# Kernel tuning notes

Measured on AMD Instinct MI355X. Metric: run time of the kernel, lower is better.

Reference implementation:

```python
import jax, jax.numpy as jnp
import numpy as np

N = 10000          # num nodes
E = 160000         # num edges (avg degree 16)
F = 128            # num_features
S = 4              # num_species
RAD = 8            # radial_embedding_dim
RO = 16            # readout_mlp_irreps = 16x0e
EPS = 0.17677669529663687  # epsilon = 1/sqrt(avg_degree)
ACT_NORM = 1.679177        # normalize_function(silu): 1/sqrt(E[silu(x)^2]), x~N(0,1)


def nsilu(x):
    return jax.nn.silu(x) * ACT_NORM


def setup_inputs() -> dict:
    key = jax.random.key(0)
    ks = jax.random.split(key, 24)
    d = {}
    d["vectors"] = jax.random.normal(ks[0], (E, 3), jnp.float32)
    d["node_scalars"] = jax.random.normal(ks[1], (N, F), jnp.float32)
    d["node_vectors"] = jax.random.normal(ks[2], (N, F, 3), jnp.float32)
    d["radial_embeddings"] = jax.random.normal(ks[3], (E, RAD), jnp.float32)
    # linear_up (irrep-wise linear on 0e and 1o)
    d["W_up_s"] = jax.random.normal(ks[4], (F, F), jnp.float32)
    d["W_up_v"] = jax.random.normal(ks[5], (F, F), jnp.float32)
    # radial MLP [RAD,64,64,64,weight_dim=4F]
    d["W_mlp1"] = jax.random.normal(ks[6], (RAD, 64), jnp.float32) / np.sqrt(RAD)
    d["b_mlp1"] = jnp.zeros((64,), jnp.float32)
    d["W_mlp2"] = jax.random.normal(ks[7], (64, 64), jnp.float32) / np.sqrt(64.0)
    d["b_mlp2"] = jnp.zeros((64,), jnp.float32)
    d["W_mlp3"] = jax.random.normal(ks[8], (64, 64), jnp.float32) / np.sqrt(64.0)
    d["b_mlp3"] = jnp.zeros((64,), jnp.float32)
    d["W_mlp4"] = jax.random.normal(ks[9], (64, 4 * F), jnp.float32) / np.sqrt(64.0)
    d["b_mlp4"] = jnp.zeros((4 * F,), jnp.float32)
    # linear_down: TP out (2F x 0e + 2F x 1o) -> F x (0e+1o)
    d["W_down_s"] = jax.random.normal(ks[10], (2 * F, F), jnp.float32)
    d["W_down_v"] = jax.random.normal(ks[11], (2 * F, F), jnp.float32)
    # species-indexed skip linear (output is hidden_out = 0e only, since last=True)
    d["Wz_s"] = jax.random.normal(ks[12], (S, F, F), jnp.float32)
    # symmetric contraction weights: 5 invariant basis terms per channel per species
    d["W_sc"] = jax.random.normal(ks[13], (S, 5, F), jnp.float32)
    d["W_post"] = jax.random.normal(ks[14], (F, F), jnp.float32)
    d["W_ro1"] = jax.random.normal(ks[15], (F, RO), jnp.float32)
    d["W_ro2"] = jax.random.normal(ks[16], (RO, 1), jnp.float32)
    d["senders"] = jax.random.randint(ks[17], (E,), 0, N)
    d["receivers"] = jax.random.randint(ks[18], (E,), 0, N)
    d["num_species_counts"] = jnp.full((S,), N // S, dtype=jnp.int32)
    d["num_nodes"] = N
    return d


def reference(vectors, node_scalars, node_vectors, radial_embeddings,
              W_up_s, W_up_v,
              W_mlp1, b_mlp1, W_mlp2, b_mlp2, W_mlp3, b_mlp3, W_mlp4, b_mlp4,
              W_down_s, W_down_v, Wz_s, W_sc, W_post, W_ro1, W_ro2,
              senders, receivers, num_species_counts, num_nodes):
    # spherical harmonics (max_ell=1): Y0 = 1, Y1 = unit edge vector
    rnorm = jnp.linalg.norm(vectors, axis=-1, keepdims=True)
    Y1 = vectors / (rnorm + 1e-12)                      # [E,3]

    # species index per node from counts
    i = jnp.repeat(jnp.arange(S), num_species_counts, total_repeat_length=num_nodes)

    # self connection (species-indexed linear on input scalars; hidden_out = 0e)
    self_conn = jnp.einsum('nf,nfg->ng', node_scalars, Wz_s[i]) / np.sqrt(F)

    # linear_up (irrep-wise)
    s = node_scalars @ W_up_s / np.sqrt(F)              # [N,F]
    v = jnp.einsum('nfc,fg->ngc', node_vectors, W_up_v) / np.sqrt(F)  # [N,F,3]

    # radial MLP -> per-edge channelwise TP weights, 4 paths x F channels
    h = nsilu(radial_embeddings @ W_mlp1 + b_mlp1)
    h = nsilu(h @ W_mlp2 + b_mlp2)
    h = nsilu(h @ W_mlp3 + b_mlp3)
    mix = (h @ W_mlp4 + b_mlp4).reshape(-1, 4, F)       # [E,4,F]

    # channelwise tensor product: gather sender feats, combine with sph
    sg = s[senders]                                     # [E,F]
    vg = v[senders]                                     # [E,F,3]
    m_s0 = mix[:, 0] * sg                               # 0e x 0e -> 0e
    m_s3 = mix[:, 3] * (jnp.einsum('efc,ec->ef', vg, Y1) / np.sqrt(3.0))  # 1o x 1o -> 0e
    m_v1 = mix[:, 1][..., None] * sg[..., None] * Y1[:, None, :]          # 0e x 1o -> 1o
    m_v2 = mix[:, 2][..., None] * vg                                      # 1o x 0e -> 1o
    msg_s = jnp.concatenate([m_s0, m_s3], axis=-1)      # [E,2F]
    msg_v = jnp.concatenate([m_v1, m_v2], axis=1)       # [E,2F,3]

    # scatter to receivers
    agg_s = jax.ops.segment_sum(msg_s, receivers, num_segments=num_nodes) * EPS
    agg_v = jax.ops.segment_sum(msg_v, receivers, num_segments=num_nodes) * EPS

    # linear_down: 2F -> F per irrep
    s2 = agg_s @ W_down_s / np.sqrt(2 * F)              # [N,F]
    v2 = jnp.einsum('nfc,fg->ngc', agg_v, W_down_v) / np.sqrt(2 * F)  # [N,F,3]

    # symmetric contraction (correlation<=3, output 0e): per-species weighted
    # invariant basis {s, s^2, |v|^2, s^3, s|v|^2} per channel
    vv = jnp.sum(v2 * v2, axis=-1)                      # [N,F]
    basis = jnp.stack([s2, s2 * s2, vv, s2 * s2 * s2, s2 * vv], axis=1)  # [N,5,F]
    sc = jnp.sum(W_sc[i] * basis, axis=1)               # [N,F]

    feats = sc @ W_post / np.sqrt(F) + self_conn        # [N,F]

    # readout (last=True): linear -> scalar activation -> linear
    hr = nsilu(feats @ W_ro1 / np.sqrt(F))              # [N,16]
    node_outputs = hr @ W_ro2 / np.sqrt(RO)             # [N,1]
    return (node_outputs, feats)
```

## Files before the change

kernel.cpp:

```cpp
#include <hip/hip_runtime.h>
#include <hip/hip_bf16.h>
#include <math.h>

#define N_NODES 10000
#define N_EDGES 160000
#define F 128
#define TE 128
#define HS 72

typedef _Float16 v8h __attribute__((ext_vector_type(8)));
typedef _Float16 v4h __attribute__((ext_vector_type(4)));
typedef float    v4f __attribute__((ext_vector_type(4)));

__device__ __forceinline__ float nsilu(float x) {
    return 1.679177f * (x / (1.0f + expf(-x)));
}

__device__ __forceinline__ void fma4(float4& a, float s, const float4& b) {
    a.x = fmaf(s, b.x, a.x); a.y = fmaf(s, b.y, a.y);
    a.z = fmaf(s, b.z, a.z); a.w = fmaf(s, b.w, a.w);
}

__device__ __forceinline__ int species_of(int n, const int* __restrict__ counts) {
    int c0 = counts[0];
    int c01 = c0 + counts[1];
    int c012 = c01 + counts[2];
    return (n >= c0) + (n >= c01) + (n >= c012);
}

__global__ __launch_bounds__(256) void k_count(const int* __restrict__ receivers,
                                               int* __restrict__ deg) {
    int e = blockIdx.x * 256 + threadIdx.x;
    if (e < N_EDGES) atomicAdd(&deg[receivers[e]], 1);
}

__global__ __launch_bounds__(1024) void k_scan(const int* __restrict__ deg,
                                               int* __restrict__ offs,
                                               int* __restrict__ cursor) {
    __shared__ int sums[1024];
    const int t = threadIdx.x;
    const int CH = 10;
    int base = t * CH;
    int local[CH];
    int s = 0;
    #pragma unroll
    for (int j = 0; j < CH; ++j) {
        int v = (base + j < N_NODES) ? deg[base + j] : 0;
        local[j] = s;
        s += v;
    }
    sums[t] = s;
    __syncthreads();
    for (int off = 1; off < 1024; off <<= 1) {
        int v = (t >= off) ? sums[t - off] : 0;
        __syncthreads();
        sums[t] += v;
        __syncthreads();
    }
    int carry = (t == 0) ? 0 : sums[t - 1];
    #pragma unroll
    for (int j = 0; j < CH; ++j) {
        int idx = base + j;
        if (idx < N_NODES) {
            int o = carry + local[j];
            offs[idx] = o;
            cursor[idx] = o;
        }
    }
    if (t == 1023) offs[N_NODES] = sums[1023];
}

__global__ __launch_bounds__(256) void k_fill(const int* __restrict__ receivers,
                                              int* __restrict__ cursor,
                                              int* __restrict__ eidx,
                                              float* __restrict__ vectors) {
    int e = blockIdx.x * 256 + threadIdx.x;
    if (e < N_EDGES) {
        int pos = atomicAdd(&cursor[receivers[e]], 1);
        eidx[pos] = e;
        float vx = vectors[e * 3 + 0];
        float vy = vectors[e * 3 + 1];
        float vz = vectors[e * 3 + 2];
        float rn = sqrtf(vx * vx + vy * vy + vz * vz) + 1e-12f;
        float inv = 1.0f / rn;
        vectors[e * 3 + 0] = vx * inv;
        vectors[e * 3 + 1] = vy * inv;
        vectors[e * 3 + 2] = vz * inv;
    }
}

__global__ __launch_bounds__(256) void k_prep_w(
    const float* __restrict__ W2, const float* __restrict__ W3,
    const float* __restrict__ W4, const float* __restrict__ b4,
    const float* __restrict__ Wup_s, const float* __restrict__ Wup_v,
    const float* __restrict__ Wz, const float* __restrict__ Wds,
    const float* __restrict__ Wdv, const float* __restrict__ Wpost,
    _Float16* __restrict__ W2t, _Float16* __restrict__ W3t,
    _Float16* __restrict__ W4t, float* __restrict__ b4p,
    _Float16* __restrict__ Wup_s_t, _Float16* __restrict__ Wup_v_t,
    _Float16* __restrict__ Wz_t, _Float16* __restrict__ Wds_t,
    _Float16* __restrict__ Wdv_t, _Float16* __restrict__ Wpost_t)
{
    int idx = blockIdx.x * 256 + threadIdx.x;
    if (idx < 4096) {
        int u = idx >> 6, k = idx & 63;
        W2t[idx] = (_Float16)W2[k * 64 + u];
    } else if (idx < 8192) {
        int j = idx - 4096;
        int u = j >> 6, k = j & 63;
        W3t[j] = (_Float16)W3[k * 64 + u];
    } else if (idx < 40960) {
        int j = idx - 8192;
        int gn = j >> 6, k = j & 63;
        int go = (gn & 3) * 128 + (gn >> 2);
        W4t[j] = (_Float16)W4[k * 512 + go];
    } else if (idx < 41472) {
        int j = idx - 40960;
        int go = (j & 3) * 128 + (j >> 2);
        b4p[j] = b4[go];
    } else if (idx < 57856) {
        int j = idx - 41472;
        int g = j >> 7, f = j & 127;
        Wup_s_t[j] = (_Float16)Wup_s[f * 128 + g];
    } else if (idx < 74240) {
        int j = idx - 57856;
        int g = j >> 7, f = j & 127;
        Wup_v_t[j] = (_Float16)Wup_v[f * 128 + g];
    } else if (idx < 139776) {
        int j = idx - 74240;
        int s = j >> 14, r = j & 16383;
        int g = r >> 7, f = r & 127;
        Wz_t[j] = (_Float16)Wz[s * 16384 + f * 128 + g];
    } else if (idx < 172544) {
        int j = idx - 139776;
        int g = j >> 8, k = j & 255;
        Wds_t[j] = (_Float16)Wds[k * 128 + g];
    } else if (idx < 205312) {
        int j = idx - 172544;
        int g = j >> 8, k = j & 255;
        Wdv_t[j] = (_Float16)Wdv[k * 128 + g];
    } else if (idx < 221696) {
        int j = idx - 205312;
        int g = j >> 7, f = j & 127;
        Wpost_t[j] = (_Float16)Wpost[f * 128 + g];
    }
}

__global__ __launch_bounds__(256) void k_prep_a(
    const float* __restrict__ ns, const float* __restrict__ nv,
    _Float16* __restrict__ ns16, _Float16* __restrict__ nv16)
{
    int idx = blockIdx.x * 256 + threadIdx.x;
    if (idx < N_NODES * F) {
        ns16[idx] = (_Float16)ns[idx];
    } else {
        int j = idx - N_NODES * F;
        int row = j >> 7, f = j & 127;
        int n = row / 3, c = row - n * 3;
        nv16[j] = (_Float16)nv[((size_t)n * F + f) * 3 + c];
    }
}

template <int K>
__device__ __forceinline__ void gemm_tile(
    const _Float16* __restrict__ A, const _Float16* __restrict__ Bg,
    float* __restrict__ out, int M, int row0, float scale,
    _Float16* Bl, const int* __restrict__ counts, int sp)
{
    const int t = threadIdx.x;
    constexpr int KP = K + 8;
    __syncthreads();
    for (int idx = t; idx < 128 * (K / 8); idx += 256) {
        int g = idx / (K / 8), kk = (idx % (K / 8)) * 8;
        *(v8h*)(Bl + g * KP + kk) = *(const v8h*)(Bg + g * K + kk);
    }
    __syncthreads();

    const int lane = t & 63;
    const int w = t >> 6;
    const int c = lane & 15;
    const int q = lane >> 4;

    v4f acc[2][8];
    #pragma unroll
    for (int mi = 0; mi < 2; ++mi)
        #pragma unroll
        for (int nt = 0; nt < 8; ++nt)
            acc[mi][nt] = (v4f){0.f, 0.f, 0.f, 0.f};

    for (int ch = 0; ch < K / 32; ++ch) {
        v8h a[2];
        #pragma unroll
        for (int mi = 0; mi < 2; ++mi) {
            int r = row0 + (2 * w + mi) * 16 + c;
            r = min(r, M - 1);
            a[mi] = *(const v8h*)(A + (size_t)r * K + ch * 32 + q * 8);
        }
        #pragma unroll
        for (int nt = 0; nt < 8; ++nt) {
            v8h b = *(const v8h*)(Bl + (nt * 16 + c) * KP + ch * 32 + q * 8);
            acc[0][nt] = __builtin_amdgcn_mfma_f32_16x16x32_f16(a[0], b, acc[0][nt], 0, 0, 0);
            acc[1][nt] = __builtin_amdgcn_mfma_f32_16x16x32_f16(a[1], b, acc[1][nt], 0, 0, 0);
        }
    }
    #pragma unroll
    for (int mi = 0; mi < 2; ++mi) {
        #pragma unroll
        for (int r = 0; r < 4; ++r) {
            int row = row0 + (2 * w + mi) * 16 + q * 4 + r;
            bool ok = row < M;
            if (ok && sp >= 0) ok = (species_of(row, counts) == sp);
            if (ok) {
                float* op = out + (size_t)row * 128;
                #pragma unroll
                for (int nt = 0; nt < 8; ++nt)
                    op[nt * 16 + c] = acc[mi][nt][r] * scale;
            }
        }
    }
}

__global__ __launch_bounds__(256) void k_gemm_up(
    const _Float16* __restrict__ ns16, const _Float16* __restrict__ nv16,
    const _Float16* __restrict__ Wup_s_t, const _Float16* __restrict__ Wup_v_t,
    const _Float16* __restrict__ Wz_t, const int* __restrict__ counts,
    float* __restrict__ s_buf, float* __restrict__ v_buf, float* __restrict__ selfc)
{
    __shared__ _Float16 Bl[128 * 136];
    const int row0 = blockIdx.x * 128;
    const float isf = 0.08838834764831845f;
    if (blockIdx.y == 0) {
        if (row0 >= N_NODES) return;
        gemm_tile<128>(ns16, Wup_s_t, s_buf, N_NODES, row0, isf, Bl, counts, -1);
    } else if (blockIdx.y == 1) {
        gemm_tile<128>(nv16, Wup_v_t, v_buf, 3 * N_NODES, row0, isf, Bl, counts, -1);
    } else {
        if (row0 >= N_NODES) return;
        int sp0 = species_of(row0, counts);
        int sp1 = species_of(min(row0 + 127, N_NODES - 1), counts);
        for (int sp = sp0; sp <= sp1; ++sp)
            gemm_tile<128>(ns16, Wz_t + (size_t)sp * 16384, selfc,
                           N_NODES, row0, isf, Bl, counts, sp);
    }
}

__global__ __launch_bounds__(256) void k_gemm_down(
    const _Float16* __restrict__ agg_s16, const _Float16* __restrict__ agg_v16,
    const _Float16* __restrict__ Wds_t, const _Float16* __restrict__ Wdv_t,
    const int* __restrict__ counts,
    float* __restrict__ s2, float* __restrict__ v2)
{
    __shared__ _Float16 Bl[128 * 264];
    const int row0 = blockIdx.x * 128;
    if (blockIdx.y == 0) {
        if (row0 >= N_NODES) return;
        gemm_tile<256>(agg_s16, Wds_t, s2, N_NODES, row0, 1.0f, Bl, counts, -1);
    } else {
        gemm_tile<256>(agg_v16, Wdv_t, v2, 3 * N_NODES, row0, 1.0f, Bl, counts, -1);
    }
}

__device__ __forceinline__ void mfma_layer64(
    const _Float16* src, _Float16* dst,
    const _Float16* __restrict__ Wt, const float* __restrict__ b,
    int w, int q, int c)
{
    v8h B[4][2];
    float bias[4];
    #pragma unroll
    for (int nt = 0; nt < 4; ++nt) {
        B[nt][0] = *(const v8h*)(Wt + (nt * 16 + c) * 64 + q * 8);
        B[nt][1] = *(const v8h*)(Wt + (nt * 16 + c) * 64 + 32 + q * 8);
        bias[nt] = b[nt * 16 + c];
    }
    #pragma unroll
    for (int mi = 0; mi < 2; ++mi) {
        int mt = 2 * w + mi;
        v8h a0 = *(const v8h*)(src + (mt * 16 + c) * HS + q * 8);
        v8h a1 = *(const v8h*)(src + (mt * 16 + c) * HS + 32 + q * 8);
        #pragma unroll
        for (int nt = 0; nt < 4; ++nt) {
            v4f acc = {bias[nt], bias[nt], bias[nt], bias[nt]};
            acc = __builtin_amdgcn_mfma_f32_16x16x32_f16(a0, B[nt][0], acc, 0, 0, 0);
            acc = __builtin_amdgcn_mfma_f32_16x16x32_f16(a1, B[nt][1], acc, 0, 0, 0);
            #pragma unroll
            for (int r = 0; r < 4; ++r)
                dst[(mt * 16 + q * 4 + r) * HS + nt * 16 + c] = (_Float16)nsilu(acc[r]);
        }
    }
}

__global__ __launch_bounds__(256) void k_mlp(
    const float* __restrict__ re,
    const float* __restrict__ W1, const float* __restrict__ b1,
    const _Float16* __restrict__ W2t, const float* __restrict__ b2,
    const _Float16* __restrict__ W3t, const float* __restrict__ b3,
    const _Float16* __restrict__ W4t, const float* __restrict__ b4p,
    _Float16* __restrict__ mix)
{
    __shared__ float sre[TE * 8];
    __shared__ _Float16 hA[TE * HS];
    __shared__ _Float16 hB[TE * HS];

    const int t = threadIdx.x;
    const int e0 = blockIdx.x * TE;

    ((float4*)sre)[t] = ((const float4*)(re + (size_t)e0 * 8))[t];
    __syncthreads();

    {
        const int uslot = t & 15;
        const int egrp = t >> 4;
        const int u0 = uslot * 4;
        float4 w[8];
        #pragma unroll
        for (int k = 0; k < 8; ++k) w[k] = *(const float4*)(W1 + k * 64 + u0);
        float4 bb = *(const float4*)(b1 + u0);
        #pragma unroll
        for (int i = 0; i < 8; ++i) {
            int e = egrp + i * 16;
            const float* rp = sre + e * 8;
            float4 a = bb;
            #pragma unroll
            for (int k = 0; k < 8; ++k) fma4(a, rp[k], w[k]);
            v4h r = {(_Float16)nsilu(a.x), (_Float16)nsilu(a.y),
                     (_Float16)nsilu(a.z), (_Float16)nsilu(a.w)};
            *(v4h*)(hA + e * HS + u0) = r;
        }
    }
    __syncthreads();

    const int lane = t & 63;
    const int w = t >> 6;
    const int c = lane & 15;
    const int q = lane >> 4;

    mfma_layer64(hA, hB, W2t, b2, w, q, c);
    mfma_layer64(hB, hA, W3t, b3, w, q, c);
    __syncthreads();

    v8h B4[8][2];
    float bias4[8];
    #pragma unroll
    for (int j = 0; j < 8; ++j) {
        int g = (8 * w + j) * 16 + c;
        B4[j][0] = *(const v8h*)(W4t + g * 64 + q * 8);
        B4[j][1] = *(const v8h*)(W4t + g * 64 + 32 + q * 8);
        bias4[j] = b4p[g];
    }
    for (int mt = 0; mt < 8; ++mt) {
        v8h a0 = *(const v8h*)(hA + (mt * 16 + c) * HS + q * 8);
        v8h a1 = *(const v8h*)(hA + (mt * 16 + c) * HS + 32 + q * 8);
        size_t rowbase = (size_t)(e0 + mt * 16 + q * 4) * 512;
        #pragma unroll
        for (int j = 0; j < 8; ++j) {
            v4f acc = {bias4[j], bias4[j], bias4[j], bias4[j]};
            acc = __builtin_amdgcn_mfma_f32_16x16x32_f16(a0, B4[j][0], acc, 0, 0, 0);
            acc = __builtin_amdgcn_mfma_f32_16x16x32_f16(a1, B4[j][1], acc, 0, 0, 0);
            int gcol = (8 * w + j) * 16 + c;
            #pragma unroll
            for (int r = 0; r < 4; ++r)
                mix[rowbase + (size_t)r * 512 + gcol] = (_Float16)acc[r];
        }
    }
}

__global__ __launch_bounds__(128) void k_gather(
    const _Float16* __restrict__ mix, const float* __restrict__ vectors,
    const int* __restrict__ senders,
    const float* __restrict__ s_buf, const float* __restrict__ v_buf,
    const int* __restrict__ offs, const int* __restrict__ eidx,
    _Float16* __restrict__ agg_s16, _Float16* __restrict__ agg_v16)
{
    const int n = blockIdx.x;
    const int f = threadIdx.x;
    const int beg = offs[n], end = offs[n + 1];
    const float inv_sqrt3 = 0.5773502691896258f;

    float as0 = 0, as1 = 0;
    float av00 = 0, av01 = 0, av02 = 0, av10 = 0, av11 = 0, av12 = 0;

    for (int p = beg; p < end; ++p) {
        int e = eidx[p];
        int snd = senders[e];
        float y0 = vectors[e * 3 + 0];
        float y1 = vectors[e * 3 + 1];
        float y2 = vectors[e * 3 + 2];

        union { uint2 u; _Float16 h[4]; } mu;
        mu.u = *(const uint2*)(mix + (size_t)e * 512 + f * 4);
        float m0 = (float)mu.h[0];
        float m1 = (float)mu.h[1];
        float m2 = (float)mu.h[2];
        float m3 = (float)mu.h[3];

        float sg = s_buf[(size_t)snd * F + f];
        const float* vb = v_buf + (size_t)snd * 384;
        float vg0 = vb[f];
        float vg1 = vb[128 + f];
        float vg2 = vb[256 + f];

        as0 += m0 * sg;
        as1 += m3 * (vg0 * y0 + vg1 * y1 + vg2 * y2) * inv_sqrt3;
        float w1s = m1 * sg;
        av00 += w1s * y0; av01 += w1s * y1; av02 += w1s * y2;
        av10 += m2 * vg0; av11 += m2 * vg1; av12 += m2 * vg2;
    }
    const float SC = 0.011048543456039804f;
    agg_s16[(size_t)n * 256 + f]       = (_Float16)(as0 * SC);
    agg_s16[(size_t)n * 256 + 128 + f] = (_Float16)(as1 * SC);
    _Float16* av = agg_v16 + (size_t)n * 768;
    av[0 * 256 + f]       = (_Float16)(av00 * SC);
    av[0 * 256 + 128 + f] = (_Float16)(av10 * SC);
    av[1 * 256 + f]       = (_Float16)(av01 * SC);
    av[1 * 256 + 128 + f] = (_Float16)(av11 * SC);
    av[2 * 256 + f]       = (_Float16)(av02 * SC);
    av[2 * 256 + 128 + f] = (_Float16)(av12 * SC);
}

__global__ __launch_bounds__(256) void k_contract(
    const float* __restrict__ s2, const float* __restrict__ v2,
    const float* __restrict__ Wsc, const int* __restrict__ counts,
    _Float16* __restrict__ sc16)
{
    int idx = blockIdx.x * 256 + threadIdx.x;
    int n = idx >> 7, g = idx & 127;
    float s = s2[idx];
    const float* vp = v2 + (size_t)n * 384;
    float a0 = vp[g], a1 = vp[128 + g], a2 = vp[256 + g];
    float vv = a0 * a0 + a1 * a1 + a2 * a2;
    const float* w = Wsc + (size_t)species_of(n, counts) * 640;
    float sc = w[g] * s + w[128 + g] * (s * s) + w[256 + g] * vv
             + w[384 + g] * (s * s * s) + w[512 + g] * (s * vv);
    sc16[idx] = (_Float16)sc;
}

__global__ __launch_bounds__(256) void k_post(
    const _Float16* __restrict__ sc16, const _Float16* __restrict__ Wpost_t,
    const float* __restrict__ selfc,
    const float* __restrict__ Wro1, const float* __restrict__ Wro2,
    float* __restrict__ out)
{
    __shared__ _Float16 Bl[128 * 136];
    __shared__ float sfeat[128][132];
    __shared__ float shr[128][16];
    const int t = threadIdx.x;
    const int row0 = blockIdx.x * 128;
    const float isf = 0.08838834764831845f;

    for (int idx = t; idx < 128 * 16; idx += 256) {
        int g = idx >> 4, kk = (idx & 15) * 8;
        *(v8h*)(Bl + g * 136 + kk) = *(const v8h*)(Wpost_t + g * 128 + kk);
    }
    __syncthreads();

    const int lane = t & 63;
    const int w = t >> 6;
    const int c = lane & 15;
    const int q = lane >> 4;

    v4f acc[2][8];
    #pragma unroll
    for (int mi = 0; mi < 2; ++mi)
        #pragma unroll
        for (int nt = 0; nt < 8; ++nt)
            acc[mi][nt] = (v4f){0.f, 0.f, 0.f, 0.f};

    for (int ch = 0; ch < 4; ++ch) {
        v8h a[2];
        #pragma unroll
        for (int mi = 0; mi < 2; ++mi) {
            int r = row0 + (2 * w + mi) * 16 + c;
            r = min(r, N_NODES - 1);
            a[mi] = *(const v8h*)(sc16 + (size_t)r * 128 + ch * 32 + q * 8);
        }
        #pragma unroll
        for (int nt = 0; nt < 8; ++nt) {
            v8h b = *(const v8h*)(Bl + (nt * 16 + c) * 136 + ch * 32 + q * 8);
            acc[0][nt] = __builtin_amdgcn_mfma_f32_16x16x32_f16(a[0], b, acc[0][nt], 0, 0, 0);
            acc[1][nt] = __builtin_amdgcn_mfma_f32_16x16x32_f16(a[1], b, acc[1][nt], 0, 0, 0);
        }
    }
    #pragma unroll
    for (int mi = 0; mi < 2; ++mi) {
        #pragma unroll
        for (int r = 0; r < 4; ++r) {
            int row = row0 + (2 * w + mi) * 16 + q * 4 + r;
            int rl = (2 * w + mi) * 16 + q * 4 + r;
            if (row < N_NODES) {
                #pragma unroll
                for (int nt = 0; nt < 8; ++nt) {
                    int col = nt * 16 + c;
                    float feat = acc[mi][nt][r] * isf + selfc[(size_t)row * 128 + col];
                    out[N_NODES + (size_t)row * 128 + col] = feat;
                    sfeat[rl][col] = feat;
                }
            } else {
                #pragma unroll
                for (int nt = 0; nt < 8; ++nt) sfeat[rl][nt * 16 + c] = 0.f;
            }
        }
    }
    __syncthreads();

    for (int idx = t; idx < 2048; idx += 256) {
        int nd = idx >> 4, u = idx & 15;
        float a = 0;
        for (int f = 0; f < 128; f += 4) {
            float4 x = *(const float4*)&sfeat[nd][f];
            a += x.x * Wro1[(f + 0) * 16 + u] + x.y * Wro1[(f + 1) * 16 + u]
               + x.z * Wro1[(f + 2) * 16 + u] + x.w * Wro1[(f + 3) * 16 + u];
        }
        shr[nd][u] = nsilu(a * isf);
    }
    __syncthreads();

    if (t < 128 && row0 + t < N_NODES) {
        float a = 0;
        #pragma unroll
        for (int j = 0; j < 16; ++j) a += shr[t][j] * Wro2[j];
        out[row0 + t] = a * 0.25f;
    }
}


extern "C" void kernel_launch(void* const* d_in, const int* in_sizes, int n_in,
                              void* d_out, int out_size, void* d_ws, size_t ws_size,
                              hipStream_t stream) {
    float* vectors            = (float*)d_in[0];
    const float* node_scalars = (const float*)d_in[1];
    const float* node_vectors = (const float*)d_in[2];
    const float* radial       = (const float*)d_in[3];
    const float* W_up_s       = (const float*)d_in[4];
    const float* W_up_v       = (const float*)d_in[5];
    const float* W1 = (const float*)d_in[6];
    const float* b1 = (const float*)d_in[7];
    const float* W2 = (const float*)d_in[8];
    const float* b2 = (const float*)d_in[9];
    const float* W3 = (const float*)d_in[10];
    const float* b3 = (const float*)d_in[11];
    const float* W4 = (const float*)d_in[12];
    const float* b4 = (const float*)d_in[13];
    const float* Wds  = (const float*)d_in[14];
    const float* Wdv  = (const float*)d_in[15];
    const float* Wz   = (const float*)d_in[16];
    const float* Wsc  = (const float*)d_in[17];
    const float* Wpost= (const float*)d_in[18];
    const float* Wro1 = (const float*)d_in[19];
    const float* Wro2 = (const float*)d_in[20];
    const int* senders   = (const int*)d_in[21];
    const int* receivers = (const int*)d_in[22];
    const int* counts    = (const int*)d_in[23];
    float* out = (float*)d_out;

    const size_t NF = (size_t)N_NODES * F;

    char* base = (char*)d_ws;
    _Float16* mix = (_Float16*)base;
    float* s2   = (float*)base;
    float* v2   = s2 + NF;
    _Float16* sc16 = (_Float16*)(v2 + 3 * NF);

    char* p = base + (size_t)N_EDGES * 512 * 2;
    _Float16* ns16 = (_Float16*)p;        p += NF * 2;
    _Float16* nv16 = (_Float16*)p;        p += 3 * NF * 2;
    float* s_buf   = (float*)p;           p += NF * 4;
    float* v_buf   = (float*)p;           p += 3 * NF * 4;
    float* selfc   = (float*)p;           p += NF * 4;
    _Float16* agg_s16 = (_Float16*)p;     p += 2 * NF * 2;
    _Float16* agg_v16 = (_Float16*)p;     p += 6 * NF * 2;
    int* deg    = (int*)p;                p += N_NODES * 4;
    int* offs   = (int*)p;                p += (N_NODES + 1) * 4;
    int* cursor = (int*)p;                p += N_NODES * 4;
    int* eidx   = (int*)p;                p += N_EDGES * 4;
    _Float16* W2t = (_Float16*)p;         p += 4096 * 2;
    _Float16* W3t = (_Float16*)p;         p += 4096 * 2;
    _Float16* W4t = (_Float16*)p;         p += 32768 * 2;
    float* b4p    = (float*)p;            p += 512 * 4;
    _Float16* Wup_s_t = (_Float16*)p;     p += 16384 * 2;
    _Float16* Wup_v_t = (_Float16*)p;     p += 16384 * 2;
    _Float16* Wz_t    = (_Float16*)p;     p += 65536 * 2;
    _Float16* Wds_t   = (_Float16*)p;     p += 32768 * 2;
    _Float16* Wdv_t   = (_Float16*)p;     p += 32768 * 2;
    _Float16* Wpost_t = (_Float16*)p;     p += 16384 * 2;

    hipMemsetAsync(deg, 0, N_NODES * sizeof(int), stream);
    k_count<<<(N_EDGES + 255) / 256, 256, 0, stream>>>(receivers, deg);
    k_scan<<<1, 1024, 0, stream>>>(deg, offs, cursor);
    k_fill<<<(N_EDGES + 255) / 256, 256, 0, stream>>>(receivers, cursor, eidx, vectors);

    k_prep_w<<<866, 256, 0, stream>>>(W2, W3, W4, b4, W_up_s, W_up_v, Wz, Wds, Wdv, Wpost,
                                      W2t, W3t, W4t, b4p, Wup_s_t, Wup_v_t, Wz_t,
                                      Wds_t, Wdv_t, Wpost_t);
    k_prep_a<<<20000, 256, 0, stream>>>(node_scalars, node_vectors, ns16, nv16);

    k_gemm_up<<<dim3(235, 3), 256, 0, stream>>>(
        ns16, nv16, Wup_s_t, Wup_v_t, Wz_t, counts, s_buf, v_buf, selfc);

    k_mlp<<<N_EDGES / TE, 256, 0, stream>>>(
        radial, W1, b1, W2t, b2, W3t, b3, W4t, b4p, mix);

    k_gather<<<N_NODES, 128, 0, stream>>>(
        mix, vectors, senders, s_buf, v_buf, offs, eidx, agg_s16, agg_v16);

    k_gemm_down<<<dim3(235, 2), 256, 0, stream>>>(
        agg_s16, agg_v16, Wds_t, Wdv_t, counts, s2, v2);

    k_contract<<<(N_NODES * F) / 256, 256, 0, stream>>>(s2, v2, Wsc, counts, sc16);

    k_post<<<(N_NODES + 127) / 128, 256, 0, stream>>>(
        sc16, Wpost_t, selfc, Wro1, Wro2, out);
}
```

Before: 335.3 us.

## Write MLP outputs in CSR order and pack edge data for the gather

The fill kernel now records each edge's CSR position and writes a packed float4 (unit vector plus sender) in receiver-sorted order. The MLP kernel stages its output tile in shared memory and scatters rows to their CSR positions, so the gather reads mix contiguously with no eidx indirection. The count, weight-prep and activation-prep kernels are merged into one setup launch. In exchange the MLP does scattered row writes and adds extra barriers, and the input vectors are no longer modified in place.

```diff
diff --git a/kernel.cpp b/kernel.cpp
--- a/kernel.cpp
+++ b/kernel.cpp
@@ -7,6 +7,7 @@
 #define F 128
 #define TE 128
 #define HS 72
+#define JP2 516
 
 typedef _Float16 v8h __attribute__((ext_vector_type(8)));
 typedef _Float16 v4h __attribute__((ext_vector_type(4)));
@@ -28,10 +29,81 @@
     return (n >= c0) + (n >= c01) + (n >= c012);
 }
 
-__global__ __launch_bounds__(256) void k_count(const int* __restrict__ receivers,
-                                               int* __restrict__ deg) {
-    int e = blockIdx.x * 256 + threadIdx.x;
-    if (e < N_EDGES) atomicAdd(&deg[receivers[e]], 1);
+__global__ __launch_bounds__(256) void k_setup(
+    const int* __restrict__ receivers, int* __restrict__ deg,
+    const float* __restrict__ W2, const float* __restrict__ W3,
+    const float* __restrict__ W4, const float* __restrict__ b4,
+    const float* __restrict__ Wup_s, const float* __restrict__ Wup_v,
+    const float* __restrict__ Wz, const float* __restrict__ Wds,
+    const float* __restrict__ Wdv, const float* __restrict__ Wpost,
+    _Float16* __restrict__ W2t, _Float16* __restrict__ W3t,
+    _Float16* __restrict__ W4t, float* __restrict__ b4p,
+    _Float16* __restrict__ Wup_s_t, _Float16* __restrict__ Wup_v_t,
+    _Float16* __restrict__ Wz_t, _Float16* __restrict__ Wds_t,
+    _Float16* __restrict__ Wdv_t, _Float16* __restrict__ Wpost_t,
+    const float* __restrict__ ns, const float* __restrict__ nv,
+    _Float16* __restrict__ ns16, _Float16* __restrict__ nv16)
+{
+    int gidx = blockIdx.x * 256 + threadIdx.x;
+    if (gidx < N_EDGES) {
+        atomicAdd(&deg[receivers[gidx]], 1);
+        return;
+    }
+    int idx = gidx - N_EDGES;
+    if (idx < 221696) {
+        if (idx < 4096) {
+            int u = idx >> 6, k = idx & 63;
+            W2t[idx] = (_Float16)W2[k * 64 + u];
+        } else if (idx < 8192) {
+            int j = idx - 4096;
+            int u = j >> 6, k = j & 63;
+            W3t[j] = (_Float16)W3[k * 64 + u];
+        } else if (idx < 40960) {
+            int j = idx - 8192;
+            int gn = j >> 6, k = j & 63;
+            int go = (gn & 3) * 128 + (gn >> 2);
+            W4t[j] = (_Float16)W4[k * 512 + go];
+        } else if (idx < 41472) {
+            int j = idx - 40960;
+            int go = (j & 3) * 128 + (j >> 2);
+            b4p[j] = b4[go];
+        } else if (idx < 57856) {
+            int j = idx - 41472;
+            int g = j >> 7, f = j & 127;
+            Wup_s_t[j] = (_Float16)Wup_s[f * 128 + g];
+        } else if (idx < 74240) {
+            int j = idx - 57856;
+            int g = j >> 7, f = j & 127;
+            Wup_v_t[j] = (_Float16)Wup_v[f * 128 + g];
+        } else if (idx < 139776) {
+            int j = idx - 74240;
+            int s = j >> 14, r = j & 16383;
+            int g = r >> 7, f = r & 127;
+            Wz_t[j] = (_Float16)Wz[s * 16384 + f * 128 + g];
+        } else if (idx < 172544) {
+            int j = idx - 139776;
+            int g = j >> 8, k = j & 255;
+            Wds_t[j] = (_Float16)Wds[k * 128 + g];
+        } else if (idx < 205312) {
+            int j = idx - 172544;
+            int g = j >> 8, k = j & 255;
+            Wdv_t[j] = (_Float16)Wdv[k * 128 + g];
+        } else {
+            int j = idx - 205312;
+            int g = j >> 7, f = j & 127;
+            Wpost_t[j] = (_Float16)Wpost[f * 128 + g];
+        }
+        return;
+    }
+    int j = idx - 221696;
+    if (j < N_NODES * F) {
+        ns16[j] = (_Float16)ns[j];
+    } else if (j < 4 * N_NODES * F) {
+        int j2 = j - N_NODES * F;
+        int row = j2 >> 7, f = j2 & 127;
+        int n = row / 3, c = row - n * 3;
+        nv16[j2] = (_Float16)nv[((size_t)n * F + f) * 3 + c];
+    }
 }
 
 __global__ __launch_bounds__(1024) void k_scan(const int* __restrict__ deg,
@@ -71,93 +143,23 @@
 }
 
 __global__ __launch_bounds__(256) void k_fill(const int* __restrict__ receivers,
+                                              const int* __restrict__ senders,
+                                              const float* __restrict__ vectors,
                                               int* __restrict__ cursor,
-                                              int* __restrict__ eidx,
-                                              float* __restrict__ vectors) {
+                                              int* __restrict__ pcsr,
+                                              float4* __restrict__ yq) {
     int e = blockIdx.x * 256 + threadIdx.x;
     if (e < N_EDGES) {
         int pos = atomicAdd(&cursor[receivers[e]], 1);
-        eidx[pos] = e;
+        pcsr[e] = pos;
         float vx = vectors[e * 3 + 0];
         float vy = vectors[e * 3 + 1];
         float vz = vectors[e * 3 + 2];
-        float rn = sqrtf(vx * vx + vy * vy + vz * vz) + 1e-12f;
-        float inv = 1.0f / rn;
-        vectors[e * 3 + 0] = vx * inv;
-        vectors[e * 3 + 1] = vy * inv;
-        vectors[e * 3 + 2] = vz * inv;
-    }
-}
-
-__global__ __launch_bounds__(256) void k_prep_w(
-    const float* __restrict__ W2, const float* __restrict__ W3,
-    const float* __restrict__ W4, const float* __restrict__ b4,
-    const float* __restrict__ Wup_s, const float* __restrict__ Wup_v,
-    const float* __restrict__ Wz, const float* __restrict__ Wds,
-    const float* __restrict__ Wdv, const float* __restrict__ Wpost,
-    _Float16* __restrict__ W2t, _Float16* __restrict__ W3t,
-    _Float16* __restrict__ W4t, float* __restrict__ b4p,
-    _Float16* __restrict__ Wup_s_t, _Float16* __restrict__ Wup_v_t,
-    _Float16* __restrict__ Wz_t, _Float16* __restrict__ Wds_t,
-    _Float16* __restrict__ Wdv_t, _Float16* __restrict__ Wpost_t)
-{
-    int idx = blockIdx.x * 256 + threadIdx.x;
-    if (idx < 4096) {
-        int u = idx >> 6, k = idx & 63;
-        W2t[idx] = (_Float16)W2[k * 64 + u];
-    } else if (idx < 8192) {
-        int j = idx - 4096;
-        int u = j >> 6, k = j & 63;
-        W3t[j] = (_Float16)W3[k * 64 + u];
-    } else if (idx < 40960) {
-        int j = idx - 8192;
-        int gn = j >> 6, k = j & 63;
-        int go = (gn & 3) * 128 + (gn >> 2);
-        W4t[j] = (_Float16)W4[k * 512 + go];
-    } else if (idx < 41472) {
-        int j = idx - 40960;
-        int go = (j & 3) * 128 + (j >> 2);
-        b4p[j] = b4[go];
-    } else if (idx < 57856) {
-        int j = idx - 41472;
-        int g = j >> 7, f = j & 127;
-        Wup_s_t[j] = (_Float16)Wup_s[f * 128 + g];
-    } else if (idx < 74240) {
-        int j = idx - 57856;
-        int g = j >> 7, f = j & 127;
-        Wup_v_t[j] = (_Float16)Wup_v[f * 128 + g];
-    } else if (idx < 139776) {
-        int j = idx - 74240;
-        int s = j >> 14, r = j & 16383;
-        int g = r >> 7, f = r & 127;
-        Wz_t[j] = (_Float16)Wz[s * 16384 + f * 128 + g];
-    } else if (idx < 172544) {
-        int j = idx - 139776;
-        int g = j >> 8, k = j & 255;
-        Wds_t[j] = (_Float16)Wds[k * 128 + g];
-    } else if (idx < 205312) {
-        int j = idx - 172544;
-        int g = j >> 8, k = j & 255;
-        Wdv_t[j] = (_Float16)Wdv[k * 128 + g];
-    } else if (idx < 221696) {
-        int j = idx - 205312;
-        int g = j >> 7, f = j & 127;
-        Wpost_t[j] = (_Float16)Wpost[f * 128 + g];
-    }
-}
-
-__global__ __launch_bounds__(256) void k_prep_a(
-    const float* __restrict__ ns, const float* __restrict__ nv,
-    _Float16* __restrict__ ns16, _Float16* __restrict__ nv16)
-{
-    int idx = blockIdx.x * 256 + threadIdx.x;
-    if (idx < N_NODES * F) {
-        ns16[idx] = (_Float16)ns[idx];
-    } else {
-        int j = idx - N_NODES * F;
-        int row = j >> 7, f = j & 127;
-        int n = row / 3, c = row - n * 3;
-        nv16[j] = (_Float16)nv[((size_t)n * F + f) * 3 + c];
+        float inv = 1.0f / (sqrtf(vx * vx + vy * vy + vz * vz) + 1e-12f);
+        float4 y;
+        y.x = vx * inv; y.y = vy * inv; y.z = vz * inv;
+        y.w = __int_as_float(senders[e]);
+        yq[pos] = y;
     }
 }
 
@@ -296,16 +298,19 @@
     const _Float16* __restrict__ W2t, const float* __restrict__ b2,
     const _Float16* __restrict__ W3t, const float* __restrict__ b3,
     const _Float16* __restrict__ W4t, const float* __restrict__ b4p,
+    const int* __restrict__ pcsr,
     _Float16* __restrict__ mix)
 {
     __shared__ float sre[TE * 8];
     __shared__ _Float16 hA[TE * HS];
     __shared__ _Float16 hB[TE * HS];
+    __shared__ int spos[TE];
 
     const int t = threadIdx.x;
     const int e0 = blockIdx.x * TE;
 
     ((float4*)sre)[t] = ((const float4*)(re + (size_t)e0 * 8))[t];
+    if (t < TE) spos[t] = pcsr[e0 + t];
     __syncthreads();
 
     {
@@ -348,28 +353,38 @@
         B4[j][1] = *(const v8h*)(W4t + g * 64 + 32 + q * 8);
         bias4[j] = b4p[g];
     }
+    _Float16* stage = hB;
     for (int mt = 0; mt < 8; ++mt) {
         v8h a0 = *(const v8h*)(hA + (mt * 16 + c) * HS + q * 8);
         v8h a1 = *(const v8h*)(hA + (mt * 16 + c) * HS + 32 + q * 8);
-        size_t rowbase = (size_t)(e0 + mt * 16 + q * 4) * 512;
         #pragma unroll
         for (int j = 0; j < 8; ++j) {
             v4f acc = {bias4[j], bias4[j], bias4[j], bias4[j]};
             acc = __builtin_amdgcn_mfma_f32_16x16x32_f16(a0, B4[j][0], acc, 0, 0, 0);
             acc = __builtin_amdgcn_mfma_f32_16x16x32_f16(a1, B4[j][1], acc, 0, 0, 0);
-            int gcol = (8 * w + j) * 16 + c;
+            int col = (8 * w + j) * 16 + c;
             #pragma unroll
             for (int r = 0; r < 4; ++r)
-                mix[rowbase + (size_t)r * 512 + gcol] = (_Float16)acc[r];
-        }
+                stage[(q * 4 + r) * JP2 + col] = (_Float16)acc[r];
+        }
+        __syncthreads();
+        {
+            int row = t & 15, seg = t >> 4;
+            int pg = spos[mt * 16 + row];
+            const _Float16* sp = stage + row * JP2 + seg * 32;
+            _Float16* dp = mix + (size_t)pg * 512 + seg * 32;
+            #pragma unroll
+            for (int k = 0; k < 8; ++k)
+                *(v4h*)(dp + k * 4) = *(const v4h*)(sp + k * 4);
+        }
+        __syncthreads();
     }
 }
 
 __global__ __launch_bounds__(128) void k_gather(
-    const _Float16* __restrict__ mix, const float* __restrict__ vectors,
-    const int* __restrict__ senders,
+    const _Float16* __restrict__ mix, const float4* __restrict__ yq,
     const float* __restrict__ s_buf, const float* __restrict__ v_buf,
-    const int* __restrict__ offs, const int* __restrict__ eidx,
+    const int* __restrict__ offs,
     _Float16* __restrict__ agg_s16, _Float16* __restrict__ agg_v16)
 {
     const int n = blockIdx.x;
@@ -381,14 +396,11 @@
     float av00 = 0, av01 = 0, av02 = 0, av10 = 0, av11 = 0, av12 = 0;
 
     for (int p = beg; p < end; ++p) {
-        int e = eidx[p];
-        int snd = senders[e];
-        float y0 = vectors[e * 3 + 0];
-        float y1 = vectors[e * 3 + 1];
-        float y2 = vectors[e * 3 + 2];
+        float4 y = yq[p];
+        int snd = __float_as_int(y.w);
 
         union { uint2 u; _Float16 h[4]; } mu;
-        mu.u = *(const uint2*)(mix + (size_t)e * 512 + f * 4);
+        mu.u = *(const uint2*)(mix + (size_t)p * 512 + f * 4);
         float m0 = (float)mu.h[0];
         float m1 = (float)mu.h[1];
         float m2 = (float)mu.h[2];
@@ -401,10 +413,10 @@
         float vg2 = vb[256 + f];
 
         as0 += m0 * sg;
-        as1 += m3 * (vg0 * y0 + vg1 * y1 + vg2 * y2) * inv_sqrt3;
+        as1 += m3 * (vg0 * y.x + vg1 * y.y + vg2 * y.z) * inv_sqrt3;
         float w1s = m1 * sg;
-        av00 += w1s * y0; av01 += w1s * y1; av02 += w1s * y2;
-        av10 += m2 * vg0; av11 += m2 * vg1; av12 += m2 * vg2;
+        av00 += w1s * y.x; av01 += w1s * y.y; av02 += w1s * y.z;
+        av10 += m2 * vg0;  av11 += m2 * vg1;  av12 += m2 * vg2;
     }
     const float SC = 0.011048543456039804f;
     agg_s16[(size_t)n * 256 + f]       = (_Float16)(as0 * SC);
@@ -527,7 +539,7 @@
 extern "C" void kernel_launch(void* const* d_in, const int* in_sizes, int n_in,
                               void* d_out, int out_size, void* d_ws, size_t ws_size,
                               hipStream_t stream) {
-    float* vectors            = (float*)d_in[0];
+    const float* vectors      = (const float*)d_in[0];
     const float* node_scalars = (const float*)d_in[1];
     const float* node_vectors = (const float*)d_in[2];
     const float* radial       = (const float*)d_in[3];
@@ -562,6 +574,7 @@
     _Float16* sc16 = (_Float16*)(v2 + 3 * NF);
 
     char* p = base + (size_t)N_EDGES * 512 * 2;
+    float4* yq     = (float4*)p;          p += (size_t)N_EDGES * 16;
     _Float16* ns16 = (_Float16*)p;        p += NF * 2;
     _Float16* nv16 = (_Float16*)p;        p += 3 * NF * 2;
     float* s_buf   = (float*)p;           p += NF * 4;
@@ -569,10 +582,10 @@
     float* selfc   = (float*)p;           p += NF * 4;
     _Float16* agg_s16 = (_Float16*)p;     p += 2 * NF * 2;
     _Float16* agg_v16 = (_Float16*)p;     p += 6 * NF * 2;
+    int* pcsr   = (int*)p;                p += (size_t)N_EDGES * 4;
     int* deg    = (int*)p;                p += N_NODES * 4;
-    int* offs   = (int*)p;                p += (N_NODES + 1) * 4;
+    int* offs   = (int*)p;                p += (N_NODES + 1) * 4 + 12;
     int* cursor = (int*)p;                p += N_NODES * 4;
-    int* eidx   = (int*)p;                p += N_EDGES * 4;
     _Float16* W2t = (_Float16*)p;         p += 4096 * 2;
     _Float16* W3t = (_Float16*)p;         p += 4096 * 2;
     _Float16* W4t = (_Float16*)p;         p += 32768 * 2;
@@ -585,23 +598,25 @@
     _Float16* Wpost_t = (_Float16*)p;     p += 16384 * 2;
 
     hipMemsetAsync(deg, 0, N_NODES * sizeof(int), stream);
-    k_count<<<(N_EDGES + 255) / 256, 256, 0, stream>>>(receivers, deg);
+
+    k_setup<<<21491, 256, 0, stream>>>(
+        receivers, deg, W2, W3, W4, b4, W_up_s, W_up_v, Wz, Wds, Wdv, Wpost,
+        W2t, W3t, W4t, b4p, Wup_s_t, Wup_v_t, Wz_t, Wds_t, Wdv_t, Wpost_t,
+        node_scalars, node_vectors, ns16, nv16);
+
     k_scan<<<1, 1024, 0, stream>>>(deg, offs, cursor);
-    k_fill<<<(N_EDGES + 255) / 256, 256, 0, stream>>>(receivers, cursor, eidx, vectors);
-
-    k_prep_w<<<866, 256, 0, stream>>>(W2, W3, W4, b4, W_up_s, W_up_v, Wz, Wds, Wdv, Wpost,
-                                      W2t, W3t, W4t, b4p, Wup_s_t, Wup_v_t, Wz_t,
-                                      Wds_t, Wdv_t, Wpost_t);
-    k_prep_a<<<20000, 256, 0, stream>>>(node_scalars, node_vectors, ns16, nv16);
+
+    k_fill<<<(N_EDGES + 255) / 256, 256, 0, stream>>>(
+        receivers, senders, vectors, cursor, pcsr, yq);
 
     k_gemm_up<<<dim3(235, 3), 256, 0, stream>>>(
         ns16, nv16, Wup_s_t, Wup_v_t, Wz_t, counts, s_buf, v_buf, selfc);
 
     k_mlp<<<N_EDGES / TE, 256, 0, stream>>>(
-        radial, W1, b1, W2t, b2, W3t, b3, W4t, b4p, mix);
+        radial, W1, b1, W2t, b2, W3t, b3, W4t, b4p, pcsr, mix);
 
     k_gather<<<N_NODES, 128, 0, stream>>>(
-        mix, vectors, senders, s_buf, v_buf, offs, eidx, agg_s16, agg_v16);
+        mix, yq, s_buf, v_buf, offs, agg_s16, agg_v16);
 
     k_gemm_down<<<dim3(235, 2), 256, 0, stream>>>(
         agg_s16, agg_v16, Wds_t, Wdv_t, counts, s2, v2);
```

Result: slower. 354.8 us (+5.8%).
